# Optimization experiments

Hardware: AMD Instinct MI355X
Metric: run time of the kernel (lower is better)

## Reference

```python
import jax, jax.numpy as jnp
from jax import lax
import numpy as np

EPS = 1e-5

def lc2d(x, w, b, stride):
    # x: [B,H,W]; w: [oh,ow,kh,kw] unshared kernels; b: [oh,ow]
    oh, ow, kh, kw = w.shape
    hi = jnp.arange(oh)[:, None] * stride + jnp.arange(kh)[None, :]  # [oh,kh]
    wi = jnp.arange(ow)[:, None] * stride + jnp.arange(kw)[None, :]  # [ow,kw]
    patches = x[:, hi[:, None, :, None], wi[None, :, None, :]]  # [B,oh,ow,kh,kw]
    return jnp.einsum('bhwkl,hwkl->bhw', patches, w) + b

def ln2d(x, g, b):
    # LayerNorm over last two dims (per-sample)
    m = jnp.mean(x, axis=(-2, -1), keepdims=True)
    v = jnp.var(x, axis=(-2, -1), keepdims=True)
    return (x - m) * lax.rsqrt(v + EPS) * g + b

def maxpool2(x):
    # MaxPool2d(kernel=2, stride=2) on [B,H,W]
    return lax.reduce_window(x, -jnp.inf, lax.max, (1, 2, 2), (1, 2, 2), 'VALID')

def setup_inputs() -> dict:
    key = jax.random.key(0)
    ks = iter(jax.random.split(key, 16))
    d = {'x': jax.random.normal(next(ks), (128, 224, 224), jnp.float32)}
    layer_specs = [(109, 7), (50, 5), (48, 3), (22, 3), (20, 3), (8, 3)]
    for i, (o, k) in enumerate(layer_specs, 1):
        std = float(np.sqrt(2.0 / (k + k)))  # xavier_normal_ on a [k,k] kernel
        d[f'w{i}'] = jax.random.normal(next(ks), (o, o, k, k), jnp.float32) * std
        d[f'b{i}'] = jnp.zeros((o, o), jnp.float32)
        d[f'g{i}'] = jnp.ones((o, o), jnp.float32)
        d[f'be{i}'] = jnp.zeros((o, o), jnp.float32)
    d['fcw'] = jax.random.normal(next(ks), (1000, 64), jnp.float32) * float(np.sqrt(1.0 / 64))
    d['fcb'] = jnp.zeros((1000,), jnp.float32)
    return d

def reference(x, w1, b1, g1, be1, w2, b2, g2, be2, w3, b3, g3, be3,
              w4, b4, g4, be4, w5, b5, g5, be5, w6, b6, g6, be6, fcw, fcb):
    # dropout is inference-mode identity (p=0)
    h = ln2d(jax.nn.relu(lc2d(x, w1, b1, 2)), g1, be1)   # [B,109,109]
    h = maxpool2(h)                                       # [B,54,54]
    h = ln2d(jax.nn.relu(lc2d(h, w2, b2, 1)), g2, be2)   # [B,50,50]
    h = ln2d(jax.nn.relu(lc2d(h, w3, b3, 1)), g3, be3)   # [B,48,48]
    h = maxpool2(h)                                       # [B,24,24]
    h = ln2d(jax.nn.relu(lc2d(h, w4, b4, 1)), g4, be4)   # [B,22,22]
    h = ln2d(jax.nn.relu(lc2d(h, w5, b5, 1)), g5, be5)   # [B,20,20]
    h = maxpool2(h)                                       # [B,10,10]
    h = ln2d(jax.nn.relu(lc2d(h, w6, b6, 1)), g6, be6)   # [B,8,8]
    logits = h.reshape(h.shape[0], -1) @ fcw.T + fcb      # [B,1000]
    return jax.nn.softmax(logits, axis=1)
```

## Files before the change

kernel.cpp:

```cpp
#include <hip/hip_runtime.h>
#include <math.h>

static constexpr float kEps = 1e-5f;

__global__ __launch_bounds__(256)
void transpose_weights(const float* __restrict__ w1, const float* __restrict__ w2,
                       const float* __restrict__ w3, const float* __restrict__ w4,
                       const float* __restrict__ w5, const float* __restrict__ w6,
                       float* __restrict__ t1, float* __restrict__ t2,
                       float* __restrict__ t3, float* __restrict__ t4,
                       float* __restrict__ t5, float* __restrict__ t6)
{
    const int tid = blockIdx.x * blockDim.x + threadIdx.x;
    const int nt  = gridDim.x * blockDim.x;
    for (int i = tid; i < 49 * 109 * 112; i += nt) {
        const int kk = i / (109 * 112), r = i % (109 * 112);
        const int oh = r / 112, ow = r % 112;
        t1[i] = (ow < 109) ? w1[(oh * 109 + ow) * 49 + kk] : 0.f;
    }
    for (int i = tid; i < 25 * 50 * 52; i += nt) {
        const int kk = i / (50 * 52), r = i % (50 * 52);
        const int oh = r / 52, ow = r % 52;
        t2[i] = (ow < 50) ? w2[(oh * 50 + ow) * 25 + kk] : 0.f;
    }
    for (int i = tid; i < 9 * 2304; i += nt) {
        const int kk = i / 2304, idx = i % 2304;
        t3[i] = w3[idx * 9 + kk];
    }
    for (int i = tid; i < 9 * 22 * 24; i += nt) {
        const int kk = i / (22 * 24), r = i % (22 * 24);
        const int oh = r / 24, ow = r % 24;
        t4[i] = (ow < 22) ? w4[(oh * 22 + ow) * 9 + kk] : 0.f;
    }
    for (int i = tid; i < 9 * 400; i += nt) {
        const int kk = i / 400, idx = i % 400;
        t5[i] = w5[idx * 9 + kk];
    }
    for (int i = tid; i < 9 * 64; i += nt) {
        const int kk = i / 64, idx = i % 64;
        t6[i] = w6[idx * 9 + kk];
    }
}

__global__ __launch_bounds__(128)
void conv1(const float* __restrict__ x, const float* __restrict__ wt,
           const float* __restrict__ bias, float* __restrict__ y,
           float* __restrict__ partial)
{
    constexpr int IN = 224, OUT = 109, K = 7, RPS = 4, QPR = 28, NS = 28;
    constexpr int ROWS = (RPS - 1) * 2 + K;
    __shared__ __align__(16) float xs0[ROWS * IN];
    __shared__ __align__(16) float xs1[ROWS * IN];
    __shared__ float red[2][4];

    const int s = blockIdx.x, bp = blockIdx.y, t = threadIdx.x;
    const int b0 = 2 * bp, b1 = b0 + 1;
    const int oh0 = s * RPS, ih0 = oh0 * 2;
    const int nrows = min(ROWS, IN - ih0);
    {
        const float4* g0 = (const float4*)(x + ((size_t)b0 * IN + ih0) * IN);
        const float4* g1 = (const float4*)(x + ((size_t)b1 * IN + ih0) * IN);
        float4* s0 = (float4*)xs0;
        float4* s1 = (float4*)xs1;
        const int n4 = nrows * (IN / 4);
        for (int i = t; i < n4; i += 128) { s0[i] = g0[i]; s1[i] = g1[i]; }
    }
    __syncthreads();

    float lsum0 = 0.f, lsq0 = 0.f, lsum1 = 0.f, lsq1 = 0.f;
    if (t < RPS * QPR) {
        const int r = t / QPR, qc = t - r * QPR;
        const int oh = oh0 + r, ow0 = qc * 4;
        if (oh < OUT) {
            float acc0[4], acc1[4];
            #pragma unroll
            for (int o = 0; o < 4; ++o) {
                const float bv = (ow0 + o < OUT) ? bias[oh * OUT + ow0 + o] : 0.f;
                acc0[o] = bv; acc1[o] = bv;
            }
            const int lr0 = r * 2, c0 = ow0 * 2;
            #pragma unroll
            for (int kh = 0; kh < K; ++kh) {
                const float* p0 = xs0 + (lr0 + kh) * IN + c0;
                const float* p1 = xs1 + (lr0 + kh) * IN + c0;
                float a0[14], a1[14];
                #pragma unroll
                for (int i = 0; i < 7; ++i) {
                    const float2 v0 = *(const float2*)(p0 + 2 * i);
                    const float2 v1 = *(const float2*)(p1 + 2 * i);
                    a0[2 * i] = v0.x; a0[2 * i + 1] = v0.y;
                    a1[2 * i] = v1.x; a1[2 * i + 1] = v1.y;
                }
                #pragma unroll
                for (int kw = 0; kw < K; ++kw) {
                    const float4 w4 = *(const float4*)(wt + ((size_t)(kh * 7 + kw) * OUT + oh) * 112 + ow0);
                    acc0[0] = fmaf(a0[kw    ], w4.x, acc0[0]);  acc1[0] = fmaf(a1[kw    ], w4.x, acc1[0]);
                    acc0[1] = fmaf(a0[kw + 2], w4.y, acc0[1]);  acc1[1] = fmaf(a1[kw + 2], w4.y, acc1[1]);
                    acc0[2] = fmaf(a0[kw + 4], w4.z, acc0[2]);  acc1[2] = fmaf(a1[kw + 4], w4.z, acc1[2]);
                    acc0[3] = fmaf(a0[kw + 6], w4.w, acc0[3]);  acc1[3] = fmaf(a1[kw + 6], w4.w, acc1[3]);
                }
            }
            float4 st0, st1;
            #pragma unroll
            for (int o = 0; o < 4; ++o) {
                const float v0 = fmaxf(acc0[o], 0.f), v1 = fmaxf(acc1[o], 0.f);
                if (ow0 + o < OUT) {
                    lsum0 += v0; lsq0 = fmaf(v0, v0, lsq0);
                    lsum1 += v1; lsq1 = fmaf(v1, v1, lsq1);
                }
                (&st0.x)[o] = v0; (&st1.x)[o] = v1;
            }
            *(float4*)(y + ((size_t)b0 * OUT + oh) * 112 + ow0) = st0;
            *(float4*)(y + ((size_t)b1 * OUT + oh) * 112 + ow0) = st1;
        }
    }
    #pragma unroll
    for (int off = 32; off > 0; off >>= 1) {
        lsum0 += __shfl_down(lsum0, off, 64);  lsq0 += __shfl_down(lsq0, off, 64);
        lsum1 += __shfl_down(lsum1, off, 64);  lsq1 += __shfl_down(lsq1, off, 64);
    }
    if ((t & 63) == 0) {
        const int w = t >> 6;
        red[w][0] = lsum0; red[w][1] = lsq0; red[w][2] = lsum1; red[w][3] = lsq1;
    }
    __syncthreads();
    if (t == 0) {
        const float a = red[0][0] + red[1][0], bq = red[0][1] + red[1][1];
        const float c = red[0][2] + red[1][2], d  = red[0][3] + red[1][3];
        partial[((size_t)b0 * NS + s) * 2]     = a;
        partial[((size_t)b0 * NS + s) * 2 + 1] = bq;
        partial[((size_t)b1 * NS + s) * 2]     = c;
        partial[((size_t)b1 * NS + s) * 2 + 1] = d;
    }
}

__device__ inline float2 block_stats4(float lsum, float lsq, float invN,
                                      float (*red)[2], int t)
{
    #pragma unroll
    for (int off = 32; off > 0; off >>= 1) {
        lsum += __shfl_down(lsum, off, 64);
        lsq  += __shfl_down(lsq,  off, 64);
    }
    if ((t & 63) == 0) { red[t >> 6][0] = lsum; red[t >> 6][1] = lsq; }
    __syncthreads();
    const float s = red[0][0] + red[1][0] + red[2][0] + red[3][0];
    const float q = red[0][1] + red[1][1] + red[2][1] + red[3][1];
    const float m = s * invN;
    return make_float2(m, rsqrtf(q * invN - m * m + kEps));
}

__global__ __launch_bounds__(256)
void tail(const float* __restrict__ y1, const float* __restrict__ partial,
          const float* __restrict__ g1, const float* __restrict__ be1,
          const float* __restrict__ w2t, const float* __restrict__ b2,
          const float* __restrict__ g2, const float* __restrict__ be2,
          const float* __restrict__ w3t, const float* __restrict__ b3,
          const float* __restrict__ g3, const float* __restrict__ be3,
          const float* __restrict__ w4t, const float* __restrict__ b4,
          const float* __restrict__ g4, const float* __restrict__ be4,
          const float* __restrict__ w5t, const float* __restrict__ b5,
          const float* __restrict__ g5, const float* __restrict__ be5,
          const float* __restrict__ w6t, const float* __restrict__ b6,
          const float* __restrict__ g6, const float* __restrict__ be6,
          const float* __restrict__ fcw, const float* __restrict__ fcb,
          float* __restrict__ out)
{
    constexpr int NS = 28;
    __shared__ __align__(16) float xs54[54 * 54 + 8];
    __shared__ __align__(16) float y50[50 * 52];
    __shared__ __align__(16) float y48[48 * 48];
    __shared__ __align__(16) float xs24[24 * 24 + 8];
    __shared__ __align__(16) float y22[22 * 24];
    __shared__ __align__(16) float y20[20 * 20];
    __shared__ __align__(16) float xs10[100];
    __shared__ float y8[64], h[64];
    __shared__ float logits[1000];
    __shared__ float red[4][2];
    __shared__ float stat[2];

    const int b = blockIdx.x, t = threadIdx.x;

    {
        float s = 0.f, q = 0.f;
        if (t < NS) {
            const float2 p = *(const float2*)(partial + ((size_t)b * NS + t) * 2);
            s = p.x; q = p.y;
        }
        if (t < 64) {
            #pragma unroll
            for (int off = 32; off > 0; off >>= 1) {
                s += __shfl_down(s, off, 64);
                q += __shfl_down(q, off, 64);
            }
            if (t == 0) {
                const float m = s / 11881.f;
                stat[0] = m;
                stat[1] = rsqrtf(q / 11881.f - m * m + kEps);
            }
        }
    }
    __syncthreads();
    const float m1 = stat[0], r1 = stat[1];

    const float* yb = y1 + (size_t)b * 109 * 112;
    #pragma unroll
    for (int it = 0; it < 12; ++it) {
        const int idx = t + it * 256;
        if (idx < 54 * 54) {
            const int ph = idx / 54, pw = idx - ph * 54;
            const int r0 = 2 * ph, c0 = 2 * pw;
            const float2 u0 = *(const float2*)(yb + r0 * 112 + c0);
            const float2 u1 = *(const float2*)(yb + (r0 + 1) * 112 + c0);
            const int i00 = r0 * 109 + c0, i10 = i00 + 109;
            const float v0 = (u0.x - m1) * r1 * g1[i00]     + be1[i00];
            const float v1 = (u0.y - m1) * r1 * g1[i00 + 1] + be1[i00 + 1];
            const float v2 = (u1.x - m1) * r1 * g1[i10]     + be1[i10];
            const float v3 = (u1.y - m1) * r1 * g1[i10 + 1] + be1[i10 + 1];
            xs54[ph * 54 + pw] = fmaxf(fmaxf(v0, v1), fmaxf(v2, v3));
        }
    }
    __syncthreads();

    float ls = 0.f, lq = 0.f;
    #pragma unroll
    for (int it = 0; it < 3; ++it) {
        const int task = t + it * 256;
        if (task < 650) {
            const int oh = task / 13, qc = task - oh * 13;
            const int ow0 = qc * 4;
            float acc[4];
            #pragma unroll
            for (int o = 0; o < 4; ++o) acc[o] = (ow0 + o < 50) ? b2[oh * 50 + ow0 + o] : 0.f;
            #pragma unroll
            for (int kh = 0; kh < 5; ++kh) {
                const float* xp = xs54 + (oh + kh) * 54 + ow0;
                float a[8];
                #pragma unroll
                for (int i = 0; i < 4; ++i) {
                    const float2 v = *(const float2*)(xp + 2 * i);
                    a[2 * i] = v.x; a[2 * i + 1] = v.y;
                }
                #pragma unroll
                for (int kw = 0; kw < 5; ++kw) {
                    const float4 w4 = *(const float4*)(w2t + ((size_t)(kh * 5 + kw) * 50 + oh) * 52 + ow0);
                    acc[0] = fmaf(a[kw    ], w4.x, acc[0]);
                    acc[1] = fmaf(a[kw + 1], w4.y, acc[1]);
                    acc[2] = fmaf(a[kw + 2], w4.z, acc[2]);
                    acc[3] = fmaf(a[kw + 3], w4.w, acc[3]);
                }
            }
            #pragma unroll
            for (int o = 0; o < 4; ++o) {
                const float v = fmaxf(acc[o], 0.f);
                y50[oh * 52 + ow0 + o] = v;
                if (ow0 + o < 50) { ls += v; lq = fmaf(v, v, lq); }
            }
        }
    }
    const float2 s2 = block_stats4(ls, lq, 1.f / 2500.f, red, t);

    #pragma unroll
    for (int it = 0; it < 10; ++it) {
        const int idx = t + it * 256;
        if (idx < 2500) {
            const int oh = idx / 50, ow = idx - oh * 50;
            const int p = oh * 52 + ow;
            y50[p] = (y50[p] - s2.x) * s2.y * g2[idx] + be2[idx];
        }
    }
    __syncthreads();

    ls = 0.f; lq = 0.f;
    #pragma unroll
    for (int it = 0; it < 3; ++it) {
        const int task = t + it * 256;
        if (task < 576) {
            const int oh = task / 12, qc = task - oh * 12;
            const int ow0 = qc * 4;
            float acc[4];
            #pragma unroll
            for (int o = 0; o < 4; ++o) acc[o] = b3[oh * 48 + ow0 + o];
            #pragma unroll
            for (int kh = 0; kh < 3; ++kh) {
                const float* xp = y50 + (oh + kh) * 52 + ow0;
                float a[6];
                #pragma unroll
                for (int i = 0; i < 3; ++i) {
                    const float2 v = *(const float2*)(xp + 2 * i);
                    a[2 * i] = v.x; a[2 * i + 1] = v.y;
                }
                #pragma unroll
                for (int kw = 0; kw < 3; ++kw) {
                    const float4 w4 = *(const float4*)(w3t + (size_t)(kh * 3 + kw) * 2304 + oh * 48 + ow0);
                    acc[0] = fmaf(a[kw    ], w4.x, acc[0]);
                    acc[1] = fmaf(a[kw + 1], w4.y, acc[1]);
                    acc[2] = fmaf(a[kw + 2], w4.z, acc[2]);
                    acc[3] = fmaf(a[kw + 3], w4.w, acc[3]);
                }
            }
            float4 st;
            #pragma unroll
            for (int o = 0; o < 4; ++o) {
                const float v = fmaxf(acc[o], 0.f);
                (&st.x)[o] = v; ls += v; lq = fmaf(v, v, lq);
            }
            *(float4*)(y48 + oh * 48 + ow0) = st;
        }
    }
    const float2 s3 = block_stats4(ls, lq, 1.f / 2304.f, red, t);

    #pragma unroll
    for (int it = 0; it < 3; ++it) {
        const int idx = t + it * 256;
        if (idx < 576) {
            const int ph = idx / 24, pw = idx - ph * 24;
            const int r0 = 2 * ph, c0 = 2 * pw;
            const float2 u0 = *(const float2*)(y48 + r0 * 48 + c0);
            const float2 u1 = *(const float2*)(y48 + (r0 + 1) * 48 + c0);
            const int i00 = r0 * 48 + c0, i10 = i00 + 48;
            const float v0 = (u0.x - s3.x) * s3.y * g3[i00]     + be3[i00];
            const float v1 = (u0.y - s3.x) * s3.y * g3[i00 + 1] + be3[i00 + 1];
            const float v2 = (u1.x - s3.x) * s3.y * g3[i10]     + be3[i10];
            const float v3 = (u1.y - s3.x) * s3.y * g3[i10 + 1] + be3[i10 + 1];
            xs24[ph * 24 + pw] = fmaxf(fmaxf(v0, v1), fmaxf(v2, v3));
        }
    }
    __syncthreads();

    ls = 0.f; lq = 0.f;
    if (t < 132) {
        const int oh = t / 6, qc = t - oh * 6;
        const int ow0 = qc * 4;
        float acc[4];
        #pragma unroll
        for (int o = 0; o < 4; ++o) acc[o] = (ow0 + o < 22) ? b4[oh * 22 + ow0 + o] : 0.f;
        #pragma unroll
        for (int kh = 0; kh < 3; ++kh) {
            const float* xp = xs24 + (oh + kh) * 24 + ow0;
            float a[6];
            #pragma unroll
            for (int i = 0; i < 3; ++i) {
                const float2 v = *(const float2*)(xp + 2 * i);
                a[2 * i] = v.x; a[2 * i + 1] = v.y;
            }
            #pragma unroll
            for (int kw = 0; kw < 3; ++kw) {
                const float4 w4 = *(const float4*)(w4t + ((size_t)(kh * 3 + kw) * 22 + oh) * 24 + ow0);
                acc[0] = fmaf(a[kw    ], w4.x, acc[0]);
                acc[1] = fmaf(a[kw + 1], w4.y, acc[1]);
                acc[2] = fmaf(a[kw + 2], w4.z, acc[2]);
                acc[3] = fmaf(a[kw + 3], w4.w, acc[3]);
            }
        }
        #pragma unroll
        for (int o = 0; o < 4; ++o) {
            const float v = fmaxf(acc[o], 0.f);
            y22[oh * 24 + ow0 + o] = v;
            if (ow0 + o < 22) { ls += v; lq = fmaf(v, v, lq); }
        }
    }
    const float2 s4 = block_stats4(ls, lq, 1.f / 484.f, red, t);

    #pragma unroll
    for (int it = 0; it < 2; ++it) {
        const int idx = t + it * 256;
        if (idx < 484) {
            const int oh = idx / 22, ow = idx - oh * 22;
            const int p = oh * 24 + ow;
            y22[p] = (y22[p] - s4.x) * s4.y * g4[idx] + be4[idx];
        }
    }
    __syncthreads();

    ls = 0.f; lq = 0.f;
    if (t < 100) {
        const int oh = t / 5, qc = t - oh * 5;
        const int ow0 = qc * 4;
        float acc[4];
        #pragma unroll
        for (int o = 0; o < 4; ++o) acc[o] = b5[oh * 20 + ow0 + o];
        #pragma unroll
        for (int kh = 0; kh < 3; ++kh) {
            const float* xp = y22 + (oh + kh) * 24 + ow0;
            float a[6];
            #pragma unroll
            for (int i = 0; i < 3; ++i) {
                const float2 v = *(const float2*)(xp + 2 * i);
                a[2 * i] = v.x; a[2 * i + 1] = v.y;
            }
            #pragma unroll
            for (int kw = 0; kw < 3; ++kw) {
                const float4 w4 = *(const float4*)(w5t + (size_t)(kh * 3 + kw) * 400 + oh * 20 + ow0);
                acc[0] = fmaf(a[kw    ], w4.x, acc[0]);
                acc[1] = fmaf(a[kw + 1], w4.y, acc[1]);
                acc[2] = fmaf(a[kw + 2], w4.z, acc[2]);
                acc[3] = fmaf(a[kw + 3], w4.w, acc[3]);
            }
        }
        #pragma unroll
        for (int o = 0; o < 4; ++o) {
            const float v = fmaxf(acc[o], 0.f);
            y20[oh * 20 + ow0 + o] = v;
            ls += v; lq = fmaf(v, v, lq);
        }
    }
    const float2 s5 = block_stats4(ls, lq, 1.f / 400.f, red, t);

    if (t < 100) {
        const int ph = t / 10, pw = t - ph * 10;
        const int r0 = 2 * ph, c0 = 2 * pw;
        const float2 u0 = *(const float2*)(y20 + r0 * 20 + c0);
        const float2 u1 = *(const float2*)(y20 + (r0 + 1) * 20 + c0);
        const int i00 = r0 * 20 + c0, i10 = i00 + 20;
        const float v0 = (u0.x - s5.x) * s5.y * g5[i00]     + be5[i00];
        const float v1 = (u0.y - s5.x) * s5.y * g5[i00 + 1] + be5[i00 + 1];
        const float v2 = (u1.x - s5.x) * s5.y * g5[i10]     + be5[i10];
        const float v3 = (u1.y - s5.x) * s5.y * g5[i10 + 1] + be5[i10 + 1];
        xs10[ph * 10 + pw] = fmaxf(fmaxf(v0, v1), fmaxf(v2, v3));
    }
    __syncthreads();

    ls = 0.f; lq = 0.f;
    if (t < 16) {
        const int oh = t / 2, qc = t - oh * 2;
        const int ow0 = qc * 4;
        float acc[4];
        #pragma unroll
        for (int o = 0; o < 4; ++o) acc[o] = b6[oh * 8 + ow0 + o];
        #pragma unroll
        for (int kh = 0; kh < 3; ++kh) {
            const float* xp = xs10 + (oh + kh) * 10 + ow0;
            float a[6];
            #pragma unroll
            for (int i = 0; i < 3; ++i) {
                const float2 v = *(const float2*)(xp + 2 * i);
                a[2 * i] = v.x; a[2 * i + 1] = v.y;
            }
            #pragma unroll
            for (int kw = 0; kw < 3; ++kw) {
                const float4 w4 = *(const float4*)(w6t + (size_t)(kh * 3 + kw) * 64 + oh * 8 + ow0);
                acc[0] = fmaf(a[kw    ], w4.x, acc[0]);
                acc[1] = fmaf(a[kw + 1], w4.y, acc[1]);
                acc[2] = fmaf(a[kw + 2], w4.z, acc[2]);
                acc[3] = fmaf(a[kw + 3], w4.w, acc[3]);
            }
        }
        #pragma unroll
        for (int o = 0; o < 4; ++o) {
            const float v = fmaxf(acc[o], 0.f);
            y8[oh * 8 + ow0 + o] = v;
            ls += v; lq = fmaf(v, v, lq);
        }
    }
    const float2 s6 = block_stats4(ls, lq, 1.f / 64.f, red, t);

    if (t < 64) h[t] = (y8[t] - s6.x) * s6.y * g6[t] + be6[t];
    __syncthreads();

    #pragma unroll
    for (int it = 0; it < 4; ++it) {
        const int j = t + it * 256;
        if (j < 1000) {
            const float4* wr = (const float4*)(fcw + (size_t)j * 64);
            float acc = fcb[j];
            #pragma unroll
            for (int k = 0; k < 16; ++k) {
                const float4 w4 = wr[k];
                acc = fmaf(h[4 * k], w4.x,
                      fmaf(h[4 * k + 1], w4.y,
                      fmaf(h[4 * k + 2], w4.z,
                      fmaf(h[4 * k + 3], w4.w, acc))));
            }
            logits[j] = acc;
        }
    }
    __syncthreads();

    float lmax = -INFINITY;
    #pragma unroll
    for (int it = 0; it < 4; ++it) {
        const int j = t + it * 256;
        if (j < 1000) lmax = fmaxf(lmax, logits[j]);
    }
    #pragma unroll
    for (int off = 32; off > 0; off >>= 1) lmax = fmaxf(lmax, __shfl_down(lmax, off, 64));
    if ((t & 63) == 0) red[t >> 6][0] = lmax;
    __syncthreads();
    const float gmax = fmaxf(fmaxf(red[0][0], red[1][0]), fmaxf(red[2][0], red[3][0]));
    __syncthreads();
    float lsum = 0.f;
    #pragma unroll
    for (int it = 0; it < 4; ++it) {
        const int j = t + it * 256;
        if (j < 1000) {
            const float e = __expf(logits[j] - gmax);
            logits[j] = e;
            lsum += e;
        }
    }
    #pragma unroll
    for (int off = 32; off > 0; off >>= 1) lsum += __shfl_down(lsum, off, 64);
    if ((t & 63) == 0) red[t >> 6][0] = lsum;
    __syncthreads();
    const float inv = 1.f / (red[0][0] + red[1][0] + red[2][0] + red[3][0]);
    #pragma unroll
    for (int it = 0; it < 4; ++it) {
        const int j = t + it * 256;
        if (j < 1000) out[(size_t)b * 1000 + j] = logits[j] * inv;
    }
}

extern "C" void kernel_launch(void* const* d_in, const int* in_sizes, int n_in,
                              void* d_out, int out_size, void* d_ws, size_t ws_size,
                              hipStream_t stream) {
    const float* x   = (const float*)d_in[0];
    const float* w1  = (const float*)d_in[1];
    const float* b1  = (const float*)d_in[2];
    const float* g1  = (const float*)d_in[3];
    const float* be1 = (const float*)d_in[4];
    const float* w2  = (const float*)d_in[5];
    const float* b2  = (const float*)d_in[6];
    const float* g2  = (const float*)d_in[7];
    const float* be2 = (const float*)d_in[8];
    const float* w3  = (const float*)d_in[9];
    const float* b3  = (const float*)d_in[10];
    const float* g3  = (const float*)d_in[11];
    const float* be3 = (const float*)d_in[12];
    const float* w4  = (const float*)d_in[13];
    const float* b4  = (const float*)d_in[14];
    const float* g4  = (const float*)d_in[15];
    const float* be4 = (const float*)d_in[16];
    const float* w5  = (const float*)d_in[17];
    const float* b5  = (const float*)d_in[18];
    const float* g5  = (const float*)d_in[19];
    const float* be5 = (const float*)d_in[20];
    const float* w6  = (const float*)d_in[21];
    const float* b6  = (const float*)d_in[22];
    const float* g6  = (const float*)d_in[23];
    const float* be6 = (const float*)d_in[24];
    const float* fcw = (const float*)d_in[25];
    const float* fcb = (const float*)d_in[26];

    float* y1p  = (float*)d_ws;
    float* w1t  = y1p  + 1562624;
    float* w2t  = w1t  + 598192;
    float* w3t  = w2t  + 65000;
    float* w4t  = w3t  + 20736;
    float* w5t  = w4t  + 4752;
    float* w6t  = w5t  + 3600;
    float* part = w6t  + 576;

    transpose_weights<<<512, 256, 0, stream>>>(w1, w2, w3, w4, w5, w6,
                                               w1t, w2t, w3t, w4t, w5t, w6t);

    conv1<<<dim3(28, 64), 128, 0, stream>>>(x, w1t, b1, y1p, part);

    tail<<<128, 256, 0, stream>>>(y1p, part, g1, be1,
                                  w2t, b2, g2, be2,
                                  w3t, b3, g3, be3,
                                  w4t, b4, g4, be4,
                                  w5t, b5, g5, be5,
                                  w6t, b6, g6, be6,
                                  fcw, fcb, (float*)d_out);
}
```

Baseline: 54.66 us.

## Widen tail kernel to 1024 threads and move small weight transposes into conv1

The tail kernel now runs 1024 threads per block, so each conv/LN stage uses one pass per thread instead of looping. The FC and softmax keep logits in registers instead of shared memory. The transposes for weights 2-6 and a 2x2-packed gamma/beta for LN1 now run in an extra row of conv1 blocks, which shortens the standalone transpose kernel and lets the first tail stage read float4 parameters. In exchange, the tail blocks are larger and more threads sit idle in the later small stages.

```diff
diff --git a/kernel.cpp b/kernel.cpp
--- a/kernel.cpp
+++ b/kernel.cpp
@@ -4,12 +4,7 @@
 static constexpr float kEps = 1e-5f;
 
 __global__ __launch_bounds__(256)
-void transpose_weights(const float* __restrict__ w1, const float* __restrict__ w2,
-                       const float* __restrict__ w3, const float* __restrict__ w4,
-                       const float* __restrict__ w5, const float* __restrict__ w6,
-                       float* __restrict__ t1, float* __restrict__ t2,
-                       float* __restrict__ t3, float* __restrict__ t4,
-                       float* __restrict__ t5, float* __restrict__ t6)
+void transpose_w1(const float* __restrict__ w1, float* __restrict__ t1)
 {
     const int tid = blockIdx.x * blockDim.x + threadIdx.x;
     const int nt  = gridDim.x * blockDim.x;
@@ -18,34 +13,20 @@
         const int oh = r / 112, ow = r % 112;
         t1[i] = (ow < 109) ? w1[(oh * 109 + ow) * 49 + kk] : 0.f;
     }
-    for (int i = tid; i < 25 * 50 * 52; i += nt) {
-        const int kk = i / (50 * 52), r = i % (50 * 52);
-        const int oh = r / 52, ow = r % 52;
-        t2[i] = (ow < 50) ? w2[(oh * 50 + ow) * 25 + kk] : 0.f;
-    }
-    for (int i = tid; i < 9 * 2304; i += nt) {
-        const int kk = i / 2304, idx = i % 2304;
-        t3[i] = w3[idx * 9 + kk];
-    }
-    for (int i = tid; i < 9 * 22 * 24; i += nt) {
-        const int kk = i / (22 * 24), r = i % (22 * 24);
-        const int oh = r / 24, ow = r % 24;
-        t4[i] = (ow < 22) ? w4[(oh * 22 + ow) * 9 + kk] : 0.f;
-    }
-    for (int i = tid; i < 9 * 400; i += nt) {
-        const int kk = i / 400, idx = i % 400;
-        t5[i] = w5[idx * 9 + kk];
-    }
-    for (int i = tid; i < 9 * 64; i += nt) {
-        const int kk = i / 64, idx = i % 64;
-        t6[i] = w6[idx * 9 + kk];
-    }
 }
 
 __global__ __launch_bounds__(128)
 void conv1(const float* __restrict__ x, const float* __restrict__ wt,
            const float* __restrict__ bias, float* __restrict__ y,
-           float* __restrict__ partial)
+           float* __restrict__ partial,
+           const float* __restrict__ w2, const float* __restrict__ w3,
+           const float* __restrict__ w4, const float* __restrict__ w5,
+           const float* __restrict__ w6,
+           const float* __restrict__ g1, const float* __restrict__ be1,
+           float* __restrict__ w2t, float* __restrict__ w3t,
+           float* __restrict__ w4t, float* __restrict__ w5t,
+           float* __restrict__ w6t,
+           float4* __restrict__ g1p, float4* __restrict__ be1p)
 {
     constexpr int IN = 224, OUT = 109, K = 7, RPS = 4, QPR = 28, NS = 28;
     constexpr int ROWS = (RPS - 1) * 2 + K;
@@ -54,16 +35,51 @@
     __shared__ float red[2][4];
 
     const int s = blockIdx.x, bp = blockIdx.y, t = threadIdx.x;
+
+    if (bp == 64) {
+        const int tid = s * 128 + t;
+        const int nt  = 28 * 128;
+        for (int i = tid; i < 25 * 50 * 52; i += nt) {
+            const int kk = i / (50 * 52), r = i % (50 * 52);
+            const int oh = r / 52, ow = r % 52;
+            w2t[i] = (ow < 50) ? w2[(oh * 50 + ow) * 25 + kk] : 0.f;
+        }
+        for (int i = tid; i < 9 * 2304; i += nt) {
+            const int kk = i / 2304, idx = i % 2304;
+            w3t[i] = w3[idx * 9 + kk];
+        }
+        for (int i = tid; i < 9 * 22 * 24; i += nt) {
+            const int kk = i / (22 * 24), r = i % (22 * 24);
+            const int oh = r / 24, ow = r % 24;
+            w4t[i] = (ow < 22) ? w4[(oh * 22 + ow) * 9 + kk] : 0.f;
+        }
+        for (int i = tid; i < 9 * 400; i += nt) {
+            const int kk = i / 400, idx = i % 400;
+            w5t[i] = w5[idx * 9 + kk];
+        }
+        for (int i = tid; i < 9 * 64; i += nt) {
+            const int kk = i / 64, idx = i % 64;
+            w6t[i] = w6[idx * 9 + kk];
+        }
+        for (int i = tid; i < 54 * 54; i += nt) {
+            const int ph = i / 54, pw = i - ph * 54;
+            const int i00 = (2 * ph) * 109 + 2 * pw, i10 = i00 + 109;
+            g1p[i]  = make_float4(g1[i00],  g1[i00 + 1],  g1[i10],  g1[i10 + 1]);
+            be1p[i] = make_float4(be1[i00], be1[i00 + 1], be1[i10], be1[i10 + 1]);
+        }
+        return;
+    }
+
     const int b0 = 2 * bp, b1 = b0 + 1;
     const int oh0 = s * RPS, ih0 = oh0 * 2;
     const int nrows = min(ROWS, IN - ih0);
     {
         const float4* g0 = (const float4*)(x + ((size_t)b0 * IN + ih0) * IN);
-        const float4* g1 = (const float4*)(x + ((size_t)b1 * IN + ih0) * IN);
+        const float4* g1r = (const float4*)(x + ((size_t)b1 * IN + ih0) * IN);
         float4* s0 = (float4*)xs0;
         float4* s1 = (float4*)xs1;
         const int n4 = nrows * (IN / 4);
-        for (int i = t; i < n4; i += 128) { s0[i] = g0[i]; s1[i] = g1[i]; }
+        for (int i = t; i < n4; i += 128) { s0[i] = g0[i]; s1[i] = g1r[i]; }
     }
     __syncthreads();
 
@@ -134,25 +150,25 @@
     }
 }
 
-__device__ inline float2 block_stats4(float lsum, float lsq, float invN,
-                                      float (*red)[2], int t)
+__device__ inline float2 bstats(float ls, float lq, float invN, float (*red)[2], int t)
 {
     #pragma unroll
     for (int off = 32; off > 0; off >>= 1) {
-        lsum += __shfl_down(lsum, off, 64);
-        lsq  += __shfl_down(lsq,  off, 64);
-    }
-    if ((t & 63) == 0) { red[t >> 6][0] = lsum; red[t >> 6][1] = lsq; }
-    __syncthreads();
-    const float s = red[0][0] + red[1][0] + red[2][0] + red[3][0];
-    const float q = red[0][1] + red[1][1] + red[2][1] + red[3][1];
+        ls += __shfl_down(ls, off, 64);
+        lq += __shfl_down(lq, off, 64);
+    }
+    if ((t & 63) == 0) { red[t >> 6][0] = ls; red[t >> 6][1] = lq; }
+    __syncthreads();
+    float s = 0.f, q = 0.f;
+    #pragma unroll
+    for (int w = 0; w < 16; ++w) { s += red[w][0]; q += red[w][1]; }
     const float m = s * invN;
     return make_float2(m, rsqrtf(q * invN - m * m + kEps));
 }
 
-__global__ __launch_bounds__(256)
+__global__ __launch_bounds__(1024)
 void tail(const float* __restrict__ y1, const float* __restrict__ partial,
-          const float* __restrict__ g1, const float* __restrict__ be1,
+          const float4* __restrict__ g1p, const float4* __restrict__ be1p,
           const float* __restrict__ w2t, const float* __restrict__ b2,
           const float* __restrict__ g2, const float* __restrict__ be2,
           const float* __restrict__ w3t, const float* __restrict__ b3,
@@ -166,7 +182,6 @@
           const float* __restrict__ fcw, const float* __restrict__ fcb,
           float* __restrict__ out)
 {
-    constexpr int NS = 28;
     __shared__ __align__(16) float xs54[54 * 54 + 8];
     __shared__ __align__(16) float y50[50 * 52];
     __shared__ __align__(16) float y48[48 * 48];
@@ -175,94 +190,81 @@
     __shared__ __align__(16) float y20[20 * 20];
     __shared__ __align__(16) float xs10[100];
     __shared__ float y8[64], h[64];
-    __shared__ float logits[1000];
-    __shared__ float red[4][2];
-    __shared__ float stat[2];
+    __shared__ float red[16][2];
 
     const int b = blockIdx.x, t = threadIdx.x;
-
-    {
-        float s = 0.f, q = 0.f;
-        if (t < NS) {
-            const float2 p = *(const float2*)(partial + ((size_t)b * NS + t) * 2);
-            s = p.x; q = p.y;
-        }
-        if (t < 64) {
-            #pragma unroll
-            for (int off = 32; off > 0; off >>= 1) {
-                s += __shfl_down(s, off, 64);
-                q += __shfl_down(q, off, 64);
-            }
-            if (t == 0) {
-                const float m = s / 11881.f;
-                stat[0] = m;
-                stat[1] = rsqrtf(q / 11881.f - m * m + kEps);
-            }
-        }
-    }
-    __syncthreads();
-    const float m1 = stat[0], r1 = stat[1];
+    const int lane = t & 63;
+
+    float s = 0.f, q = 0.f;
+    if (lane < 28) {
+        const float2 p = *(const float2*)(partial + ((size_t)b * 28 + lane) * 2);
+        s = p.x; q = p.y;
+    }
+    #pragma unroll
+    for (int off = 32; off > 0; off >>= 1) {
+        s += __shfl_down(s, off, 64);
+        q += __shfl_down(q, off, 64);
+    }
+    s = __shfl(s, 0, 64); q = __shfl(q, 0, 64);
+    const float m1 = s / 11881.f;
+    const float r1 = rsqrtf(q / 11881.f - m1 * m1 + kEps);
 
     const float* yb = y1 + (size_t)b * 109 * 112;
     #pragma unroll
-    for (int it = 0; it < 12; ++it) {
-        const int idx = t + it * 256;
+    for (int it = 0; it < 3; ++it) {
+        const int idx = t + it * 1024;
         if (idx < 54 * 54) {
             const int ph = idx / 54, pw = idx - ph * 54;
             const int r0 = 2 * ph, c0 = 2 * pw;
             const float2 u0 = *(const float2*)(yb + r0 * 112 + c0);
             const float2 u1 = *(const float2*)(yb + (r0 + 1) * 112 + c0);
-            const int i00 = r0 * 109 + c0, i10 = i00 + 109;
-            const float v0 = (u0.x - m1) * r1 * g1[i00]     + be1[i00];
-            const float v1 = (u0.y - m1) * r1 * g1[i00 + 1] + be1[i00 + 1];
-            const float v2 = (u1.x - m1) * r1 * g1[i10]     + be1[i10];
-            const float v3 = (u1.y - m1) * r1 * g1[i10 + 1] + be1[i10 + 1];
+            const float4 g = g1p[idx], be = be1p[idx];
+            const float v0 = (u0.x - m1) * r1 * g.x + be.x;
+            const float v1 = (u0.y - m1) * r1 * g.y + be.y;
+            const float v2 = (u1.x - m1) * r1 * g.z + be.z;
+            const float v3 = (u1.y - m1) * r1 * g.w + be.w;
             xs54[ph * 54 + pw] = fmaxf(fmaxf(v0, v1), fmaxf(v2, v3));
         }
     }
     __syncthreads();
 
     float ls = 0.f, lq = 0.f;
+    if (t < 650) {
+        const int oh = t / 13, qc = t - oh * 13;
+        const int ow0 = qc * 4;
+        float acc[4];
+        #pragma unroll
+        for (int o = 0; o < 4; ++o) acc[o] = (ow0 + o < 50) ? b2[oh * 50 + ow0 + o] : 0.f;
+        #pragma unroll
+        for (int kh = 0; kh < 5; ++kh) {
+            const float* xp = xs54 + (oh + kh) * 54 + ow0;
+            float a[8];
+            #pragma unroll
+            for (int i = 0; i < 4; ++i) {
+                const float2 v = *(const float2*)(xp + 2 * i);
+                a[2 * i] = v.x; a[2 * i + 1] = v.y;
+            }
+            #pragma unroll
+            for (int kw = 0; kw < 5; ++kw) {
+                const float4 w4 = *(const float4*)(w2t + ((size_t)(kh * 5 + kw) * 50 + oh) * 52 + ow0);
+                acc[0] = fmaf(a[kw    ], w4.x, acc[0]);
+                acc[1] = fmaf(a[kw + 1], w4.y, acc[1]);
+                acc[2] = fmaf(a[kw + 2], w4.z, acc[2]);
+                acc[3] = fmaf(a[kw + 3], w4.w, acc[3]);
+            }
+        }
+        #pragma unroll
+        for (int o = 0; o < 4; ++o) {
+            const float v = fmaxf(acc[o], 0.f);
+            y50[oh * 52 + ow0 + o] = v;
+            if (ow0 + o < 50) { ls += v; lq = fmaf(v, v, lq); }
+        }
+    }
+    const float2 s2 = bstats(ls, lq, 1.f / 2500.f, red, t);
+
     #pragma unroll
     for (int it = 0; it < 3; ++it) {
-        const int task = t + it * 256;
-        if (task < 650) {
-            const int oh = task / 13, qc = task - oh * 13;
-            const int ow0 = qc * 4;
-            float acc[4];
-            #pragma unroll
-            for (int o = 0; o < 4; ++o) acc[o] = (ow0 + o < 50) ? b2[oh * 50 + ow0 + o] : 0.f;
-            #pragma unroll
-            for (int kh = 0; kh < 5; ++kh) {
-                const float* xp = xs54 + (oh + kh) * 54 + ow0;
-                float a[8];
-                #pragma unroll
-                for (int i = 0; i < 4; ++i) {
-                    const float2 v = *(const float2*)(xp + 2 * i);
-                    a[2 * i] = v.x; a[2 * i + 1] = v.y;
-                }
-                #pragma unroll
-                for (int kw = 0; kw < 5; ++kw) {
-                    const float4 w4 = *(const float4*)(w2t + ((size_t)(kh * 5 + kw) * 50 + oh) * 52 + ow0);
-                    acc[0] = fmaf(a[kw    ], w4.x, acc[0]);
-                    acc[1] = fmaf(a[kw + 1], w4.y, acc[1]);
-                    acc[2] = fmaf(a[kw + 2], w4.z, acc[2]);
-                    acc[3] = fmaf(a[kw + 3], w4.w, acc[3]);
-                }
-            }
-            #pragma unroll
-            for (int o = 0; o < 4; ++o) {
-                const float v = fmaxf(acc[o], 0.f);
-                y50[oh * 52 + ow0 + o] = v;
-                if (ow0 + o < 50) { ls += v; lq = fmaf(v, v, lq); }
-            }
-        }
-    }
-    const float2 s2 = block_stats4(ls, lq, 1.f / 2500.f, red, t);
-
-    #pragma unroll
-    for (int it = 0; it < 10; ++it) {
-        const int idx = t + it * 256;
+        const int idx = t + it * 1024;
         if (idx < 2500) {
             const int oh = idx / 50, ow = idx - oh * 50;
             const int p = oh * 52 + ow;
@@ -272,59 +274,51 @@
     __syncthreads();
 
     ls = 0.f; lq = 0.f;
-    #pragma unroll
-    for (int it = 0; it < 3; ++it) {
-        const int task = t + it * 256;
-        if (task < 576) {
-            const int oh = task / 12, qc = task - oh * 12;
-            const int ow0 = qc * 4;
-            float acc[4];
-            #pragma unroll
-            for (int o = 0; o < 4; ++o) acc[o] = b3[oh * 48 + ow0 + o];
-            #pragma unroll
-            for (int kh = 0; kh < 3; ++kh) {
-                const float* xp = y50 + (oh + kh) * 52 + ow0;
-                float a[6];
-                #pragma unroll
-                for (int i = 0; i < 3; ++i) {
-                    const float2 v = *(const float2*)(xp + 2 * i);
-                    a[2 * i] = v.x; a[2 * i + 1] = v.y;
-                }
-                #pragma unroll
-                for (int kw = 0; kw < 3; ++kw) {
-                    const float4 w4 = *(const float4*)(w3t + (size_t)(kh * 3 + kw) * 2304 + oh * 48 + ow0);
-                    acc[0] = fmaf(a[kw    ], w4.x, acc[0]);
-                    acc[1] = fmaf(a[kw + 1], w4.y, acc[1]);
-                    acc[2] = fmaf(a[kw + 2], w4.z, acc[2]);
-                    acc[3] = fmaf(a[kw + 3], w4.w, acc[3]);
-                }
-            }
-            float4 st;
-            #pragma unroll
-            for (int o = 0; o < 4; ++o) {
-                const float v = fmaxf(acc[o], 0.f);
-                (&st.x)[o] = v; ls += v; lq = fmaf(v, v, lq);
-            }
-            *(float4*)(y48 + oh * 48 + ow0) = st;
-        }
-    }
-    const float2 s3 = block_stats4(ls, lq, 1.f / 2304.f, red, t);
-
-    #pragma unroll
-    for (int it = 0; it < 3; ++it) {
-        const int idx = t + it * 256;
-        if (idx < 576) {
-            const int ph = idx / 24, pw = idx - ph * 24;
-            const int r0 = 2 * ph, c0 = 2 * pw;
-            const float2 u0 = *(const float2*)(y48 + r0 * 48 + c0);
-            const float2 u1 = *(const float2*)(y48 + (r0 + 1) * 48 + c0);
-            const int i00 = r0 * 48 + c0, i10 = i00 + 48;
-            const float v0 = (u0.x - s3.x) * s3.y * g3[i00]     + be3[i00];
-            const float v1 = (u0.y - s3.x) * s3.y * g3[i00 + 1] + be3[i00 + 1];
-            const float v2 = (u1.x - s3.x) * s3.y * g3[i10]     + be3[i10];
-            const float v3 = (u1.y - s3.x) * s3.y * g3[i10 + 1] + be3[i10 + 1];
-            xs24[ph * 24 + pw] = fmaxf(fmaxf(v0, v1), fmaxf(v2, v3));
-        }
+    if (t < 576) {
+        const int oh = t / 12, qc = t - oh * 12;
+        const int ow0 = qc * 4;
+        float acc[4];
+        #pragma unroll
+        for (int o = 0; o < 4; ++o) acc[o] = b3[oh * 48 + ow0 + o];
+        #pragma unroll
+        for (int kh = 0; kh < 3; ++kh) {
+            const float* xp = y50 + (oh + kh) * 52 + ow0;
+            float a[6];
+            #pragma unroll
+            for (int i = 0; i < 3; ++i) {
+                const float2 v = *(const float2*)(xp + 2 * i);
+                a[2 * i] = v.x; a[2 * i + 1] = v.y;
+            }
+            #pragma unroll
+            for (int kw = 0; kw < 3; ++kw) {
+                const float4 w4 = *(const float4*)(w3t + (size_t)(kh * 3 + kw) * 2304 + oh * 48 + ow0);
+                acc[0] = fmaf(a[kw    ], w4.x, acc[0]);
+                acc[1] = fmaf(a[kw + 1], w4.y, acc[1]);
+                acc[2] = fmaf(a[kw + 2], w4.z, acc[2]);
+                acc[3] = fmaf(a[kw + 3], w4.w, acc[3]);
+            }
+        }
+        float4 st;
+        #pragma unroll
+        for (int o = 0; o < 4; ++o) {
+            const float v = fmaxf(acc[o], 0.f);
+            (&st.x)[o] = v; ls += v; lq = fmaf(v, v, lq);
+        }
+        *(float4*)(y48 + oh * 48 + ow0) = st;
+    }
+    const float2 s3 = bstats(ls, lq, 1.f / 2304.f, red, t);
+
+    if (t < 576) {
+        const int ph = t / 24, pw = t - ph * 24;
+        const int r0 = 2 * ph, c0 = 2 * pw;
+        const float2 u0 = *(const float2*)(y48 + r0 * 48 + c0);
+        const float2 u1 = *(const float2*)(y48 + (r0 + 1) * 48 + c0);
+        const int i00 = r0 * 48 + c0, i10 = i00 + 48;
+        const float v0 = (u0.x - s3.x) * s3.y * g3[i00]     + be3[i00];
+        const float v1 = (u0.y - s3.x) * s3.y * g3[i00 + 1] + be3[i00 + 1];
+        const float v2 = (u1.x - s3.x) * s3.y * g3[i10]     + be3[i10];
+        const float v3 = (u1.y - s3.x) * s3.y * g3[i10 + 1] + be3[i10 + 1];
+        xs24[ph * 24 + pw] = fmaxf(fmaxf(v0, v1), fmaxf(v2, v3));
     }
     __syncthreads();
 
@@ -360,16 +354,12 @@
             if (ow0 + o < 22) { ls += v; lq = fmaf(v, v, lq); }
         }
     }
-    const float2 s4 = block_stats4(ls, lq, 1.f / 484.f, red, t);
-
-    #pragma unroll
-    for (int it = 0; it < 2; ++it) {
-        const int idx = t + it * 256;
-        if (idx < 484) {
-            const int oh = idx / 22, ow = idx - oh * 22;
-            const int p = oh * 24 + ow;
-            y22[p] = (y22[p] - s4.x) * s4.y * g4[idx] + be4[idx];
-        }
+    const float2 s4 = bstats(ls, lq, 1.f / 484.f, red, t);
+
+    if (t < 484) {
+        const int oh = t / 22, ow = t - oh * 22;
+        const int p = oh * 24 + ow;
+        y22[p] = (y22[p] - s4.x) * s4.y * g4[t] + be4[t];
     }
     __syncthreads();
 
@@ -405,7 +395,7 @@
             ls += v; lq = fmaf(v, v, lq);
         }
     }
-    const float2 s5 = block_stats4(ls, lq, 1.f / 400.f, red, t);
+    const float2 s5 = bstats(ls, lq, 1.f / 400.f, red, t);
 
     if (t < 100) {
         const int ph = t / 10, pw = t - ph * 10;
@@ -453,62 +443,44 @@
             ls += v; lq = fmaf(v, v, lq);
         }
     }
-    const float2 s6 = block_stats4(ls, lq, 1.f / 64.f, red, t);
+    const float2 s6 = bstats(ls, lq, 1.f / 64.f, red, t);
 
     if (t < 64) h[t] = (y8[t] - s6.x) * s6.y * g6[t] + be6[t];
     __syncthreads();
 
-    #pragma unroll
-    for (int it = 0; it < 4; ++it) {
-        const int j = t + it * 256;
-        if (j < 1000) {
-            const float4* wr = (const float4*)(fcw + (size_t)j * 64);
-            float acc = fcb[j];
-            #pragma unroll
-            for (int k = 0; k < 16; ++k) {
-                const float4 w4 = wr[k];
-                acc = fmaf(h[4 * k], w4.x,
-                      fmaf(h[4 * k + 1], w4.y,
-                      fmaf(h[4 * k + 2], w4.z,
-                      fmaf(h[4 * k + 3], w4.w, acc))));
-            }
-            logits[j] = acc;
-        }
-    }
-    __syncthreads();
-
-    float lmax = -INFINITY;
-    #pragma unroll
-    for (int it = 0; it < 4; ++it) {
-        const int j = t + it * 256;
-        if (j < 1000) lmax = fmaxf(lmax, logits[j]);
-    }
-    #pragma unroll
-    for (int off = 32; off > 0; off >>= 1) lmax = fmaxf(lmax, __shfl_down(lmax, off, 64));
-    if ((t & 63) == 0) red[t >> 6][0] = lmax;
-    __syncthreads();
-    const float gmax = fmaxf(fmaxf(red[0][0], red[1][0]), fmaxf(red[2][0], red[3][0]));
-    __syncthreads();
-    float lsum = 0.f;
-    #pragma unroll
-    for (int it = 0; it < 4; ++it) {
-        const int j = t + it * 256;
-        if (j < 1000) {
-            const float e = __expf(logits[j] - gmax);
-            logits[j] = e;
-            lsum += e;
-        }
-    }
-    #pragma unroll
-    for (int off = 32; off > 0; off >>= 1) lsum += __shfl_down(lsum, off, 64);
-    if ((t & 63) == 0) red[t >> 6][0] = lsum;
-    __syncthreads();
-    const float inv = 1.f / (red[0][0] + red[1][0] + red[2][0] + red[3][0]);
-    #pragma unroll
-    for (int it = 0; it < 4; ++it) {
-        const int j = t + it * 256;
-        if (j < 1000) out[(size_t)b * 1000 + j] = logits[j] * inv;
-    }
+    float lj = -INFINITY;
+    if (t < 1000) {
+        const float4* wr = (const float4*)(fcw + (size_t)t * 64);
+        float acc = fcb[t];
+        #pragma unroll
+        for (int k = 0; k < 16; ++k) {
+            const float4 w4 = wr[k];
+            acc = fmaf(h[4 * k], w4.x,
+                  fmaf(h[4 * k + 1], w4.y,
+                  fmaf(h[4 * k + 2], w4.z,
+                  fmaf(h[4 * k + 3], w4.w, acc))));
+        }
+        lj = acc;
+    }
+    float mx = lj;
+    #pragma unroll
+    for (int off = 32; off > 0; off >>= 1) mx = fmaxf(mx, __shfl_down(mx, off, 64));
+    if (lane == 0) red[t >> 6][0] = mx;
+    __syncthreads();
+    float gmax = red[0][0];
+    #pragma unroll
+    for (int w = 1; w < 16; ++w) gmax = fmaxf(gmax, red[w][0]);
+
+    const float e = (t < 1000) ? __expf(lj - gmax) : 0.f;
+    float ssum = e;
+    #pragma unroll
+    for (int off = 32; off > 0; off >>= 1) ssum += __shfl_down(ssum, off, 64);
+    if (lane == 0) red[t >> 6][1] = ssum;
+    __syncthreads();
+    float tot = 0.f;
+    #pragma unroll
+    for (int w = 0; w < 16; ++w) tot += red[w][1];
+    if (t < 1000) out[(size_t)b * 1000 + t] = e / tot;
 }
 
 extern "C" void kernel_launch(void* const* d_in, const int* in_sizes, int n_in,
@@ -550,17 +522,22 @@
     float* w5t  = w4t  + 4752;
     float* w6t  = w5t  + 3600;
     float* part = w6t  + 576;
-
-    transpose_weights<<<512, 256, 0, stream>>>(w1, w2, w3, w4, w5, w6,
-                                               w1t, w2t, w3t, w4t, w5t, w6t);
-
-    conv1<<<dim3(28, 64), 128, 0, stream>>>(x, w1t, b1, y1p, part);
-
-    tail<<<128, 256, 0, stream>>>(y1p, part, g1, be1,
-                                  w2t, b2, g2, be2,
-                                  w3t, b3, g3, be3,
-                                  w4t, b4, g4, be4,
-                                  w5t, b5, g5, be5,
-                                  w6t, b6, g6, be6,
-                                  fcw, fcb, (float*)d_out);
+    float* g1pp = part + 7168;
+    float* be1pp= g1pp + 11664;
+
+    transpose_w1<<<512, 256, 0, stream>>>(w1, w1t);
+
+    conv1<<<dim3(28, 65), 128, 0, stream>>>(x, w1t, b1, y1p, part,
+                                            w2, w3, w4, w5, w6, g1, be1,
+                                            w2t, w3t, w4t, w5t, w6t,
+                                            (float4*)g1pp, (float4*)be1pp);
+
+    tail<<<128, 1024, 0, stream>>>(y1p, part,
+                                   (const float4*)g1pp, (const float4*)be1pp,
+                                   w2t, b2, g2, be2,
+                                   w3t, b3, g3, be3,
+                                   w4t, b4, g4, be4,
+                                   w5t, b5, g5, be5,
+                                   w6t, b6, g6, be6,
+                                   fcw, fcb, (float*)d_out);
 }
```

After: 53.06 us. -2.9%, faster.
